# Kernel optimization log

Measured on AMD Instinct MI355X. Metric: run time of the kernel, lower is better.

Reference implementation:

```python
import jax, jax.numpy as jnp
import numpy as np

N, E = 50000, 800000
H, KC, EC, NH = 64, 64, 32, 4   # hidden, key, edge channels, heads
HPH, KPH = H // NH, KC // NH    # per-head value/key dims (16, 16)


def ssp(x):
    # ShiftedSoftplus
    return jax.nn.softplus(x) - jnp.log(2.0).astype(x.dtype)


def grouped_lin(x, w):
    # x: (N, NH, in_per_head), w: (NH, out_per_head, in_per_head)
    # equivalent to Conv1d(kernel=1, groups=NH, bias=False)
    return jnp.einsum('nhi,hoi->nho', x, w)


def lin(x, w, b):
    return x @ w.T + b


def segment_softmax(logits, seg, num_segments):
    # logits: (E, NH), seg: (E,)
    m = jax.ops.segment_max(logits, seg, num_segments=num_segments)
    m = jnp.where(jnp.isfinite(m), m, 0.0)
    e = jnp.exp(logits - m[seg])
    s = jax.ops.segment_sum(e, seg, num_segments=num_segments)
    return e / s[seg]


def setup_inputs() -> dict:
    key = jax.random.key(0)
    ks = jax.random.split(key, 24)
    sc = 0.05
    inp = {
        'x': jax.random.normal(ks[0], (N, H), jnp.float32),
        'edge_index': jax.random.randint(ks[1], (2, E), 0, N, jnp.int64),
        'edge_attr': jax.random.normal(ks[2], (E, EC), jnp.float32),
        # grouped 1x1 convs (block-diagonal linears), no bias
        'k_w': jax.random.normal(ks[3], (NH, KPH, HPH), jnp.float32) * sc,
        'q_w': jax.random.normal(ks[4], (NH, KPH, HPH), jnp.float32) * sc,
        'v_w': jax.random.normal(ks[5], (NH, HPH, HPH), jnp.float32) * sc,
        # weight_k_net: Linear(EC,KPH) -> ssp -> Linear(KPH,KPH)
        'wkn_w1': jax.random.normal(ks[6], (KPH, EC), jnp.float32) * sc,
        'wkn_b1': jnp.zeros((KPH,), jnp.float32),
        'wkn_w2': jax.random.normal(ks[7], (KPH, KPH), jnp.float32) * sc,
        'wkn_b2': jnp.zeros((KPH,), jnp.float32),
        'wkl_w': jax.random.normal(ks[8], (KPH, KPH), jnp.float32) * sc,
        'wkl_b': jnp.zeros((KPH,), jnp.float32),
        # weight_v_net: Linear(EC,HPH) -> ssp -> Linear(HPH,HPH)
        'wvn_w1': jax.random.normal(ks[9], (HPH, EC), jnp.float32) * sc,
        'wvn_b1': jnp.zeros((HPH,), jnp.float32),
        'wvn_w2': jax.random.normal(ks[10], (HPH, HPH), jnp.float32) * sc,
        'wvn_b2': jnp.zeros((HPH,), jnp.float32),
        'wvl_w': jax.random.normal(ks[11], (HPH, HPH), jnp.float32) * sc,
        'wvl_b': jnp.zeros((HPH,), jnp.float32),
        'cen_w': jax.random.normal(ks[12], (H, H), jnp.float32) * sc,
        'cen_b': jnp.zeros((H,), jnp.float32),
        'out_w': jax.random.normal(ks[13], (H, H), jnp.float32) * sc,
        'out_b': jnp.zeros((H,), jnp.float32),
    }
    return inp


def reference(x, edge_index, edge_attr, k_w, q_w, v_w,
              wkn_w1, wkn_b1, wkn_w2, wkn_b2, wkl_w, wkl_b,
              wvn_w1, wvn_b1, wvn_w2, wvn_b2, wvl_w, wvl_b,
              cen_w, cen_b, out_w, out_b):
    n = x.shape[0]
    row, col = edge_index[0], edge_index[1]
    xh = x.reshape(n, NH, HPH)                       # per-head split of channels
    h_keys = grouped_lin(xh, k_w)                    # (N, NH, KPH)
    h_queries = grouped_lin(xh, q_w)                 # (N, NH, KPH)
    h_values = grouped_lin(xh, v_w)                  # (N, NH, HPH)

    W_k = lin(ssp(lin(edge_attr, wkn_w1, wkn_b1)), wkn_w2, wkn_b2)   # (E, KPH)
    keys_j = lin(W_k[:, None, :] * h_keys[col], wkl_w, wkl_b)        # (E, NH, KPH)
    queries_i = h_queries[row]                                       # (E, NH, KPH)
    qk_ij = jnp.sum(queries_i * keys_j, axis=-1)                     # (E, NH)
    alpha = segment_softmax(qk_ij, row, n)                           # (E, NH)

    W_v = lin(ssp(lin(edge_attr, wvn_w1, wvn_b1)), wvn_w2, wvn_b2)   # (E, HPH)
    msg_j = lin(W_v[:, None, :] * h_values[col], wvl_w, wvl_b)       # (E, NH, HPH)
    msg_j = alpha[:, :, None] * msg_j
    aggr = jax.ops.segment_sum(msg_j, row, num_segments=n).reshape(n, H)

    out = lin(x, cen_w, cen_b) + aggr
    return lin(ssp(out), out_w, out_b)
```

## Files before the change

kernel.cpp:

```cpp
#include <hip/hip_runtime.h>
#include <math.h>
#include <stdint.h>

#define NN 50000
#define NE 800000
#define HD 64
#define ECH 32
#define NHEAD 4
#define NBLK 196
#define NEBLK (NE / 256)

static_assert(NE % 256 == 0, "edge kernel assumes full blocks");

typedef __attribute__((ext_vector_type(8))) short bf8;
typedef __attribute__((ext_vector_type(4))) float f32x4;
typedef __attribute__((ext_vector_type(2))) float v2f;
typedef __attribute__((ext_vector_type(2))) __bf16 v2bf;

__device__ __forceinline__ float ssp_f(float v) {
    return fmaxf(v, 0.0f) + log1pf(__expf(-fabsf(v))) - 0.69314718055994531f;
}
__device__ __forceinline__ float bf2f(uint32_t b) { return __uint_as_float(b << 16); }

__device__ __forceinline__ uint32_t cvt_pk_bf16(float lo, float hi) {
    v2f v = {lo, hi};
    v2bf b = __builtin_convertvector(v, v2bf);
    return __builtin_bit_cast(uint32_t, b);
}
__device__ __forceinline__ v2f bfpair(uint32_t p) {
    v2f r;
    r.x = __uint_as_float(p << 16);
    r.y = __uint_as_float(p & 0xffff0000u);
    return r;
}
__device__ __forceinline__ uint4 pack8c(const float* s) {
    uint4 r;
    r.x = cvt_pk_bf16(s[0], s[1]);
    r.y = cvt_pk_bf16(s[2], s[3]);
    r.z = cvt_pk_bf16(s[4], s[5]);
    r.w = cvt_pk_bf16(s[6], s[7]);
    return r;
}
__device__ __forceinline__ bf8 pack_bf8(float4 a, float4 b) {
    union { uint32_t u[4]; bf8 v; } r;
    r.u[0] = cvt_pk_bf16(a.x, a.y);
    r.u[1] = cvt_pk_bf16(a.z, a.w);
    r.u[2] = cvt_pk_bf16(b.x, b.y);
    r.u[3] = cvt_pk_bf16(b.z, b.w);
    return r.v;
}
__device__ __forceinline__ bf8 zero_bf8() {
    bf8 r;
    #pragma unroll
    for (int i = 0; i < 8; ++i) r[i] = 0;
    return r;
}

__global__ __launch_bounds__(256) void node_count_kernel(
    const float* __restrict__ x, const int* __restrict__ ei,
    const float* __restrict__ k_w, const float* __restrict__ q_w, const float* __restrict__ v_w,
    const float* __restrict__ wkl_w, const float* __restrict__ wkl_b,
    uint16_t* __restrict__ qtq, uint16_t* __restrict__ hkv,
    int* __restrict__ counts)
{
    atomicAdd(counts + ei[blockIdx.x * 256 + threadIdx.x], 1);

    if (blockIdx.x >= NBLK) return;
    __shared__ float skw[NHEAD * 256], sqw[NHEAD * 256], svw[NHEAD * 256];
    __shared__ float s_kl[256], s_klb[16];
    for (int i = threadIdx.x; i < NHEAD * 256; i += 256) {
        skw[i] = k_w[i]; sqw[i] = q_w[i]; svw[i] = v_w[i];
    }
    if (threadIdx.x < 256) s_kl[threadIdx.x] = wkl_w[threadIdx.x];
    if (threadIdx.x < 16) s_klb[threadIdx.x] = wkl_b[threadIdx.x];
    __syncthreads();
    int n = blockIdx.x * 256 + threadIdx.x;
    if (n >= NN) return;
    const float* xn = x + (size_t)n * HD;
    uint16_t* qrow = qtq + (size_t)n * 72;
    uint16_t* kvrow = hkv + (size_t)n * 128;
    float qbv[NHEAD];
    for (int h = 0; h < NHEAD; ++h) {
        v2f xr2[8];
        {
            const float4* xp = (const float4*)(xn + h * 16);
            #pragma unroll
            for (int j = 0; j < 4; ++j) {
                float4 t4 = xp[j];
                xr2[2 * j] = (v2f){t4.x, t4.y};
                xr2[2 * j + 1] = (v2f){t4.z, t4.w};
            }
        }
        float rq[16], rk[16], rv[16];
        for (int o = 0; o < 16; ++o) {
            const v2f* wq = (const v2f*)(sqw + h * 256 + o * 16);
            const v2f* wk = (const v2f*)(skw + h * 256 + o * 16);
            const v2f* wv = (const v2f*)(svw + h * 256 + o * 16);
            v2f sq = {0.f, 0.f}, sk = {0.f, 0.f}, sv = {0.f, 0.f};
            #pragma unroll
            for (int j = 0; j < 8; ++j) {
                sq += xr2[j] * wq[j];
                sk += xr2[j] * wk[j];
                sv += xr2[j] * wv[j];
            }
            rq[o] = sq.x + sq.y; rk[o] = sk.x + sk.y; rv[o] = sv.x + sv.y;
        }
        float rqt[16];
        #pragma unroll
        for (int ip = 0; ip < 8; ++ip) {
            v2f s2 = {0.f, 0.f};
            #pragma unroll
            for (int o = 0; o < 16; ++o) {
                v2f kl = *(const v2f*)(s_kl + o * 16 + 2 * ip);
                v2f q2 = {rq[o], rq[o]};
                s2 += q2 * kl;
            }
            rqt[2 * ip] = s2.x; rqt[2 * ip + 1] = s2.y;
        }
        float qbh = 0.f;
        #pragma unroll
        for (int o = 0; o < 16; ++o) qbh += rq[o] * s_klb[o];
        qbv[h] = qbh;

        uint4* oq = (uint4*)(qrow + h * 16);
        uint4* ok = (uint4*)(kvrow + h * 16);
        uint4* ov = (uint4*)(kvrow + 64 + h * 16);
        oq[0] = pack8c(rqt); oq[1] = pack8c(rqt + 8);
        ok[0] = pack8c(rk);  ok[1] = pack8c(rk + 8);
        ov[0] = pack8c(rv);  ov[1] = pack8c(rv + 8);
    }
    *(float4*)(qrow + 64) = *(float4*)&qbv[0];
}

__global__ __launch_bounds__(256) void scan_bsum_kernel(
    const int* __restrict__ counts, int* __restrict__ bsum)
{
    __shared__ int sd[256];
    int i = blockIdx.x * 256 + threadIdx.x;
    sd[threadIdx.x] = (i < NN) ? counts[i] : 0;
    __syncthreads();
    for (int s = 128; s > 0; s >>= 1) {
        if (threadIdx.x < (unsigned)s) sd[threadIdx.x] += sd[threadIdx.x + s];
        __syncthreads();
    }
    if (threadIdx.x == 0) bsum[blockIdx.x] = sd[0];
}

__global__ __launch_bounds__(256) void scan_top_kernel(int* __restrict__ bsum)
{
    __shared__ int tmp[256];
    int v = (threadIdx.x < NBLK) ? bsum[threadIdx.x] : 0;
    tmp[threadIdx.x] = v;
    __syncthreads();
    for (int d = 1; d < 256; d <<= 1) {
        int t = (threadIdx.x >= (unsigned)d) ? tmp[threadIdx.x - d] : 0;
        __syncthreads();
        tmp[threadIdx.x] += t;
        __syncthreads();
    }
    if (threadIdx.x < NBLK) bsum[threadIdx.x] = tmp[threadIdx.x] - v;
}

__global__ __launch_bounds__(256) void scan_final_kernel(
    const int* __restrict__ counts, const int* __restrict__ bsum,
    int* __restrict__ offsets, int* __restrict__ cursor)
{
    __shared__ int tmp[256];
    int i = blockIdx.x * 256 + threadIdx.x;
    int v = (i < NN) ? counts[i] : 0;
    tmp[threadIdx.x] = v;
    __syncthreads();
    for (int d = 1; d < 256; d <<= 1) {
        int t = (threadIdx.x >= (unsigned)d) ? tmp[threadIdx.x - d] : 0;
        __syncthreads();
        tmp[threadIdx.x] += t;
        __syncthreads();
    }
    int excl = tmp[threadIdx.x] - v + bsum[blockIdx.x];
    if (i < NN) { offsets[i] = excl; cursor[i] = excl; }
}

__global__ __launch_bounds__(256) void scatter_kernel(
    const int* __restrict__ ei, int* __restrict__ cursor,
    int* __restrict__ elist, int2* __restrict__ rc)
{
    int e = blockIdx.x * 256 + threadIdx.x;
    if (e >= NE) return;
    int r = ei[e];
    int c = ei[NE + e];
    int pos = atomicAdd(cursor + r, 1);
    elist[pos] = e;
    rc[pos] = make_int2(r, c);
}

__global__ __launch_bounds__(256) void edge_compute_kernel(
    const int* __restrict__ elist, const int2* __restrict__ rc,
    const float* __restrict__ ea,
    const float* __restrict__ wkn_w1, const float* __restrict__ wkn_b1,
    const float* __restrict__ wkn_w2, const float* __restrict__ wkn_b2,
    const float* __restrict__ wvn_w1, const float* __restrict__ wvn_b1,
    const float* __restrict__ wvn_w2, const float* __restrict__ wvn_b2,
    const uint16_t* __restrict__ qtq, const uint16_t* __restrict__ hkv,
    uint16_t* __restrict__ payload, float* __restrict__ wfac)
{
    __shared__ uint16_t s_trA[4][64][24];
    __shared__ uint16_t s_trB[4][64][24];

    const int w = threadIdx.x >> 6;
    const int L = threadIdx.x & 63;
    const int m = L & 15;
    const int g = L >> 4;
    const int ebase = blockIdx.x * 256 + w * 64;

    int eidv[4];
    int2 rcv[4];
    #pragma unroll
    for (int t = 0; t < 4; ++t) eidv[t] = elist[ebase + 16 * t + m];
    #pragma unroll
    for (int t = 0; t < 4; ++t) rcv[t] = rc[ebase + 16 * t + m];

    bf8 eaf[4];
    #pragma unroll
    for (int t = 0; t < 4; ++t) {
        const float* er = ea + (size_t)eidv[t] * ECH + 8 * g;
        eaf[t] = pack_bf8(*(const float4*)er, *(const float4*)(er + 4));
    }
    bf8 w1kf, w1vf, w2kf, w2vf;
    {
        const float* p = wkn_w1 + m * 32 + 8 * g;
        w1kf = pack_bf8(*(const float4*)p, *(const float4*)(p + 4));
        p = wvn_w1 + m * 32 + 8 * g;
        w1vf = pack_bf8(*(const float4*)p, *(const float4*)(p + 4));
        if (g < 2) {
            p = wkn_w2 + m * 16 + 8 * g;
            w2kf = pack_bf8(*(const float4*)p, *(const float4*)(p + 4));
            p = wvn_w2 + m * 16 + 8 * g;
            w2vf = pack_bf8(*(const float4*)p, *(const float4*)(p + 4));
        } else {
            w2kf = zero_bf8(); w2vf = zero_bf8();
        }
    }
    float4 b1k = *(const float4*)(wkn_b1 + 4 * g);
    float4 b1v = *(const float4*)(wvn_b1 + 4 * g);
    float4 b2k = *(const float4*)(wkn_b2 + 4 * g);
    float4 b2v = *(const float4*)(wvn_b2 + 4 * g);

    #pragma unroll
    for (int t = 0; t < 4; ++t) {
        f32x4 acc = {b1k.x, b1k.y, b1k.z, b1k.w};
        acc = __builtin_amdgcn_mfma_f32_16x16x32_bf16(w1kf, eaf[t], acc, 0, 0, 0);
        uint2 pk;
        pk.x = cvt_pk_bf16(ssp_f(acc[0]), ssp_f(acc[1]));
        pk.y = cvt_pk_bf16(ssp_f(acc[2]), ssp_f(acc[3]));
        *(uint2*)&s_trA[w][16 * t + m][4 * g] = pk;
    }
    bf8 l1k[4];
    #pragma unroll
    for (int t = 0; t < 4; ++t)
        l1k[t] = (g < 2) ? *(const bf8*)&s_trA[w][16 * t + m][8 * g] : zero_bf8();
    #pragma unroll
    for (int t = 0; t < 4; ++t) {
        f32x4 acc = {b1v.x, b1v.y, b1v.z, b1v.w};
        acc = __builtin_amdgcn_mfma_f32_16x16x32_bf16(w1vf, eaf[t], acc, 0, 0, 0);
        uint2 pk;
        pk.x = cvt_pk_bf16(ssp_f(acc[0]), ssp_f(acc[1]));
        pk.y = cvt_pk_bf16(ssp_f(acc[2]), ssp_f(acc[3]));
        *(uint2*)&s_trA[w][16 * t + m][4 * g] = pk;
    }
    bf8 l1v[4];
    #pragma unroll
    for (int t = 0; t < 4; ++t)
        l1v[t] = (g < 2) ? *(const bf8*)&s_trA[w][16 * t + m][8 * g] : zero_bf8();

    #pragma unroll
    for (int t = 0; t < 4; ++t) {
        f32x4 acc = {b2k.x, b2k.y, b2k.z, b2k.w};
        acc = __builtin_amdgcn_mfma_f32_16x16x32_bf16(w2kf, l1k[t], acc, 0, 0, 0);
        uint2 pk;
        pk.x = cvt_pk_bf16(acc[0], acc[1]);
        pk.y = cvt_pk_bf16(acc[2], acc[3]);
        *(uint2*)&s_trB[w][16 * t + m][4 * g] = pk;

        f32x4 accv = {b2v.x, b2v.y, b2v.z, b2v.w};
        accv = __builtin_amdgcn_mfma_f32_16x16x32_bf16(w2vf, l1v[t], accv, 0, 0, 0);
        uint2 pv;
        pv.x = cvt_pk_bf16(accv[0], accv[1]);
        pv.y = cvt_pk_bf16(accv[2], accv[3]);
        *(uint2*)&s_trA[w][16 * t + m][4 * g] = pv;
    }

    #pragma unroll
    for (int t = 0; t < 4; ++t) {
        const int E = ebase + 16 * t + m;
        const int row = rcv[t].x, col = rcv[t].y;

        uint32_t wk_u[8], wv_u[8];
        *(uint4*)&wk_u[0] = *(const uint4*)&s_trB[w][16 * t + m][0];
        *(uint4*)&wk_u[4] = *(const uint4*)&s_trB[w][16 * t + m][8];
        *(uint4*)&wv_u[0] = *(const uint4*)&s_trA[w][16 * t + m][0];
        *(uint4*)&wv_u[4] = *(const uint4*)&s_trA[w][16 * t + m][8];

        const uint16_t* qrow = qtq + (size_t)row * 72;
        const uint16_t* kvrow = hkv + (size_t)col * 128;
        uint32_t q_u[8], k_u[8], v_u[8];
        *(uint4*)&q_u[0] = *(const uint4*)(qrow + 16 * g);
        *(uint4*)&q_u[4] = *(const uint4*)(qrow + 16 * g + 8);
        *(uint4*)&k_u[0] = *(const uint4*)(kvrow + 16 * g);
        *(uint4*)&k_u[4] = *(const uint4*)(kvrow + 16 * g + 8);
        *(uint4*)&v_u[0] = *(const uint4*)(kvrow + 64 + 16 * g);
        *(uint4*)&v_u[4] = *(const uint4*)(kvrow + 64 + 16 * g + 8);

        v2f qk2 = {0.f, 0.f};
        #pragma unroll
        for (int i = 0; i < 8; ++i)
            qk2 += bfpair(q_u[i]) * (bfpair(wk_u[i]) * bfpair(k_u[i]));
        float qk = *(const float*)(qrow + 64 + 2 * g) + qk2.x + qk2.y;
        float wgt = __expf(qk);
        v2f wgt2 = {wgt, wgt};

        uint32_t po[8];
        #pragma unroll
        for (int i = 0; i < 8; ++i) {
            v2f o2 = (bfpair(wv_u[i]) * bfpair(v_u[i])) * wgt2;
            po[i] = cvt_pk_bf16(o2.x, o2.y);
        }
        uint4* pd = (uint4*)(payload + (size_t)E * HD + 16 * g);
        pd[0] = *(uint4*)&po[0];
        pd[1] = *(uint4*)&po[4];
        wfac[(size_t)E * NHEAD + g] = wgt;
    }
}

__global__ __launch_bounds__(256) void gather_finalize_kernel(
    const float* __restrict__ x,
    const uint16_t* __restrict__ payload, const float* __restrict__ wfac,
    const int* __restrict__ offsets, const int* __restrict__ counts,
    const float* __restrict__ wvl_w, const float* __restrict__ wvl_b,
    const float* __restrict__ cen_w, const float* __restrict__ cen_b,
    const float* __restrict__ out_w, const float* __restrict__ out_b,
    float* __restrict__ out)
{
    __shared__ float s_cw[4096], s_ow[4096];
    __shared__ float s_wvl[256], s_vlb[16];
    __shared__ float s_m[4][64], s_x[4][64], s_t[4][64];
    for (int idx = threadIdx.x; idx < 4096; idx += 256) {
        int o = idx & 63, i = idx >> 6;
        s_cw[i * 64 + o] = cen_w[o * 64 + i];
        s_ow[i * 64 + o] = out_w[o * 64 + i];
    }
    if (threadIdx.x < 256) s_wvl[threadIdx.x] = wvl_w[threadIdx.x];
    if (threadIdx.x < 16) s_vlb[threadIdx.x] = wvl_b[threadIdx.x];
    __syncthreads();

    int l = threadIdx.x >> 6;
    int L = threadIdx.x & 63;
    int q = L & 7;
    int g = L >> 3;
    int h = q >> 1;

    int n0 = blockIdx.x * 64 + l * 16;
    int pj = n0 + (L & 15);
    bool pvalid = pj < NN;
    int offv = 0, cntv = 0;
    if (L < 16) offv = pvalid ? offsets[pj] : 0;
    else if (L < 32) cntv = pvalid ? counts[pj] : 0;

    for (int t = 0; t < 16; ++t) {
        int n = n0 + t;
        bool valid = n < NN;
        int st = __shfl(offv, t);
        int deg = valid ? __shfl(cntv, 16 + t) : 0;
        float u[8] = {0.f, 0.f, 0.f, 0.f, 0.f, 0.f, 0.f, 0.f};
        float ds = 0.f;
        const uint16_t* pp = payload + (size_t)st * HD + 8 * q;
        const float* wp = wfac + (size_t)st * NHEAD + h;
        int iters = (deg + 7) >> 3;
        for (int i = 0; i < iters; ++i) {
            int e = 8 * i + g;
            if (e < deg) {
                uint4 pv = *(const uint4*)(pp + (size_t)e * HD);
                u[0] += bf2f(pv.x & 0xffffu); u[1] += bf2f(pv.x >> 16);
                u[2] += bf2f(pv.y & 0xffffu); u[3] += bf2f(pv.y >> 16);
                u[4] += bf2f(pv.z & 0xffffu); u[5] += bf2f(pv.z >> 16);
                u[6] += bf2f(pv.w & 0xffffu); u[7] += bf2f(pv.w >> 16);
                ds += wp[(size_t)e * NHEAD];
            }
        }
        #pragma unroll
        for (int s = 8; s < 64; s <<= 1) {
            #pragma unroll
            for (int j = 0; j < 8; ++j) u[j] += __shfl_xor(u[j], s);
            ds += __shfl_xor(ds, s);
        }
        if (g == 0) {
            float inv = (deg > 0) ? (1.f / ds) : 0.f;
            float r0[4] = {u[0] * inv, u[1] * inv, u[2] * inv, u[3] * inv};
            float r1[4] = {u[4] * inv, u[5] * inv, u[6] * inv, u[7] * inv};
            *(float4*)&s_m[l][8 * q] = *(float4*)r0;
            *(float4*)&s_m[l][8 * q + 4] = *(float4*)r1;
        }
        s_x[l][L] = valid ? x[(size_t)n * HD + L] : 0.f;

        int c = L, hh = c >> 4;
        float aggr = 0.f;
        if (deg > 0) {
            int o = c & 15;
            float s = s_vlb[o];
            #pragma unroll
            for (int i = 0; i < 16; ++i) s += s_m[l][hh * 16 + i] * s_wvl[o * 16 + i];
            aggr = s;
        }
        float sc = cen_b[c];
        #pragma unroll 8
        for (int i = 0; i < 64; ++i) sc += s_x[l][i] * s_cw[i * 64 + c];
        sc += aggr;
        s_t[l][c] = ssp_f(sc);
        float so = out_b[c];
        #pragma unroll 8
        for (int i = 0; i < 64; ++i) so += s_t[l][i] * s_ow[i * 64 + c];
        if (valid) out[(size_t)n * HD + c] = so;
    }
}

extern "C" void kernel_launch(void* const* d_in, const int* in_sizes, int n_in,
                              void* d_out, int out_size, void* d_ws, size_t ws_size,
                              hipStream_t stream)
{
    const float* x      = (const float*)d_in[0];
    const int*   ei     = (const int*)d_in[1];
    const float* ea     = (const float*)d_in[2];
    const float* k_w    = (const float*)d_in[3];
    const float* q_w    = (const float*)d_in[4];
    const float* v_w    = (const float*)d_in[5];
    const float* wkn_w1 = (const float*)d_in[6];
    const float* wkn_b1 = (const float*)d_in[7];
    const float* wkn_w2 = (const float*)d_in[8];
    const float* wkn_b2 = (const float*)d_in[9];
    const float* wkl_w  = (const float*)d_in[10];
    const float* wkl_b  = (const float*)d_in[11];
    const float* wvn_w1 = (const float*)d_in[12];
    const float* wvn_b1 = (const float*)d_in[13];
    const float* wvn_w2 = (const float*)d_in[14];
    const float* wvn_b2 = (const float*)d_in[15];
    const float* wvl_w  = (const float*)d_in[16];
    const float* wvl_b  = (const float*)d_in[17];
    const float* cen_w  = (const float*)d_in[18];
    const float* cen_b  = (const float*)d_in[19];
    const float* out_w  = (const float*)d_in[20];
    const float* out_b  = (const float*)d_in[21];
    float* out = (float*)d_out;

    float* wfac  = (float*)d_ws;
    uint16_t* qtq = (uint16_t*)(wfac + (size_t)NE * NHEAD);
    uint16_t* hkv = qtq + (size_t)NN * 72;
    uint16_t* payload = hkv + (size_t)NN * 128;
    int2* rc     = (int2*)(payload + (size_t)NE * HD);
    int* elist   = (int*)(rc + (size_t)NE);
    int* counts  = elist + NE;
    int* bsum    = counts + NN;
    int* offsets = bsum + 256;
    int* cursor  = offsets + NN;

    hipMemsetAsync(counts, 0, (size_t)NN * sizeof(int), stream);
    node_count_kernel<<<NEBLK, 256, 0, stream>>>(
        x, ei, k_w, q_w, v_w, wkl_w, wkl_b, qtq, hkv, counts);
    scan_bsum_kernel<<<NBLK, 256, 0, stream>>>(counts, bsum);
    scan_top_kernel<<<1, 256, 0, stream>>>(bsum);
    scan_final_kernel<<<NBLK, 256, 0, stream>>>(counts, bsum, offsets, cursor);
    scatter_kernel<<<NEBLK, 256, 0, stream>>>(ei, cursor, elist, rc);
    edge_compute_kernel<<<NEBLK, 256, 0, stream>>>(
        elist, rc, ea, wkn_w1, wkn_b1, wkn_w2, wkn_b2,
        wvn_w1, wvn_b1, wvn_w2, wvn_b2,
        qtq, hkv, payload, wfac);
    gather_finalize_kernel<<<(NN + 63) / 64, 256, 0, stream>>>(
        x, payload, wfac, offsets, counts,
        wvl_w, wvl_b, cen_w, cen_b, out_w, out_b, out);
}
```

Before: 474.7 us.

## Split gather_finalize into a wave-per-node gather kernel and separate finalize kernel

```diff
diff --git a/kernel.cpp b/kernel.cpp
--- a/kernel.cpp
+++ b/kernel.cpp
@@ -331,91 +331,110 @@
     }
 }
 
-__global__ __launch_bounds__(256) void gather_finalize_kernel(
-    const float* __restrict__ x,
+__global__ __launch_bounds__(256) void gather_kernel(
     const uint16_t* __restrict__ payload, const float* __restrict__ wfac,
     const int* __restrict__ offsets, const int* __restrict__ counts,
+    float* __restrict__ mout)
+{
+    const int n = (blockIdx.x * 256 + threadIdx.x) >> 6;
+    if (n >= NN) return;
+    const int L = threadIdx.x & 63;
+    const int q = L & 7;
+    const int g = L >> 3;
+    const int h = q >> 1;
+
+    const int st = offsets[n];
+    const int deg = counts[n];
+
+    v2f u2[4] = {{0.f,0.f},{0.f,0.f},{0.f,0.f},{0.f,0.f}};
+    float ds = 0.f;
+    const uint16_t* pp = payload + (size_t)st * HD + 8 * q;
+    const float* wp = wfac + (size_t)st * NHEAD + h;
+    const int iters = (deg + 7) >> 3;
+    for (int i = 0; i < iters; i += 2) {
+        const int e0 = 8 * i + g;
+        const int e1 = e0 + 8;
+        if (e0 < deg) {
+            uint4 pv = *(const uint4*)(pp + (size_t)e0 * HD);
+            u2[0] += bfpair(pv.x); u2[1] += bfpair(pv.y);
+            u2[2] += bfpair(pv.z); u2[3] += bfpair(pv.w);
+            ds += wp[(size_t)e0 * NHEAD];
+        }
+        if (e1 < deg) {
+            uint4 pv = *(const uint4*)(pp + (size_t)e1 * HD);
+            u2[0] += bfpair(pv.x); u2[1] += bfpair(pv.y);
+            u2[2] += bfpair(pv.z); u2[3] += bfpair(pv.w);
+            ds += wp[(size_t)e1 * NHEAD];
+        }
+    }
+    #pragma unroll
+    for (int s = 8; s < 64; s <<= 1) {
+        #pragma unroll
+        for (int j = 0; j < 4; ++j) {
+            u2[j].x += __shfl_xor(u2[j].x, s);
+            u2[j].y += __shfl_xor(u2[j].y, s);
+        }
+        ds += __shfl_xor(ds, s);
+    }
+    if (g == 0) {
+        float inv = (deg > 0) ? (1.f / ds) : 0.f;
+        float r0[4] = {u2[0].x * inv, u2[0].y * inv, u2[1].x * inv, u2[1].y * inv};
+        float r1[4] = {u2[2].x * inv, u2[2].y * inv, u2[3].x * inv, u2[3].y * inv};
+        float* mr = mout + (size_t)n * HD + 8 * q;
+        *(float4*)mr = *(float4*)r0;
+        *(float4*)(mr + 4) = *(float4*)r1;
+    }
+}
+
+__global__ __launch_bounds__(256) void finalize_kernel(
+    const float* __restrict__ x, const float* __restrict__ m,
+    const int* __restrict__ counts,
     const float* __restrict__ wvl_w, const float* __restrict__ wvl_b,
     const float* __restrict__ cen_w, const float* __restrict__ cen_b,
     const float* __restrict__ out_w, const float* __restrict__ out_b,
     float* __restrict__ out)
 {
     __shared__ float s_cw[4096], s_ow[4096];
-    __shared__ float s_wvl[256], s_vlb[16];
-    __shared__ float s_m[4][64], s_x[4][64], s_t[4][64];
+    __shared__ float s_x[4][64], s_m[4][64], s_t[4][64];
     for (int idx = threadIdx.x; idx < 4096; idx += 256) {
         int o = idx & 63, i = idx >> 6;
         s_cw[i * 64 + o] = cen_w[o * 64 + i];
         s_ow[i * 64 + o] = out_w[o * 64 + i];
     }
-    if (threadIdx.x < 256) s_wvl[threadIdx.x] = wvl_w[threadIdx.x];
-    if (threadIdx.x < 16) s_vlb[threadIdx.x] = wvl_b[threadIdx.x];
     __syncthreads();
 
-    int l = threadIdx.x >> 6;
-    int L = threadIdx.x & 63;
-    int q = L & 7;
-    int g = L >> 3;
-    int h = q >> 1;
-
-    int n0 = blockIdx.x * 64 + l * 16;
-    int pj = n0 + (L & 15);
-    bool pvalid = pj < NN;
-    int offv = 0, cntv = 0;
-    if (L < 16) offv = pvalid ? offsets[pj] : 0;
-    else if (L < 32) cntv = pvalid ? counts[pj] : 0;
-
+    const int l = threadIdx.x >> 6;
+    const int c = threadIdx.x & 63;
+    const int hh = c >> 4;
+
+    float wvlr[16];
+    #pragma unroll
+    for (int i = 0; i < 16; ++i) wvlr[i] = wvl_w[(c & 15) * 16 + i];
+    const float vlb = wvl_b[c & 15];
+    const float cb = cen_b[c];
+    const float ob = out_b[c];
+
+    const int n0 = blockIdx.x * 64 + l * 16;
     for (int t = 0; t < 16; ++t) {
-        int n = n0 + t;
-        bool valid = n < NN;
-        int st = __shfl(offv, t);
-        int deg = valid ? __shfl(cntv, 16 + t) : 0;
-        float u[8] = {0.f, 0.f, 0.f, 0.f, 0.f, 0.f, 0.f, 0.f};
-        float ds = 0.f;
-        const uint16_t* pp = payload + (size_t)st * HD + 8 * q;
-        const float* wp = wfac + (size_t)st * NHEAD + h;
-        int iters = (deg + 7) >> 3;
-        for (int i = 0; i < iters; ++i) {
-            int e = 8 * i + g;
-            if (e < deg) {
-                uint4 pv = *(const uint4*)(pp + (size_t)e * HD);
-                u[0] += bf2f(pv.x & 0xffffu); u[1] += bf2f(pv.x >> 16);
-                u[2] += bf2f(pv.y & 0xffffu); u[3] += bf2f(pv.y >> 16);
-                u[4] += bf2f(pv.z & 0xffffu); u[5] += bf2f(pv.z >> 16);
-                u[6] += bf2f(pv.w & 0xffffu); u[7] += bf2f(pv.w >> 16);
-                ds += wp[(size_t)e * NHEAD];
-            }
-        }
-        #pragma unroll
-        for (int s = 8; s < 64; s <<= 1) {
-            #pragma unroll
-            for (int j = 0; j < 8; ++j) u[j] += __shfl_xor(u[j], s);
-            ds += __shfl_xor(ds, s);
-        }
-        if (g == 0) {
-            float inv = (deg > 0) ? (1.f / ds) : 0.f;
-            float r0[4] = {u[0] * inv, u[1] * inv, u[2] * inv, u[3] * inv};
-            float r1[4] = {u[4] * inv, u[5] * inv, u[6] * inv, u[7] * inv};
-            *(float4*)&s_m[l][8 * q] = *(float4*)r0;
-            *(float4*)&s_m[l][8 * q + 4] = *(float4*)r1;
-        }
-        s_x[l][L] = valid ? x[(size_t)n * HD + L] : 0.f;
-
-        int c = L, hh = c >> 4;
+        const int n = n0 + t;
+        const bool valid = n < NN;
+        const int deg = valid ? counts[n] : 0;
+        s_x[l][c] = valid ? x[(size_t)n * HD + c] : 0.f;
+        s_m[l][c] = valid ? m[(size_t)n * HD + c] : 0.f;
+
         float aggr = 0.f;
         if (deg > 0) {
-            int o = c & 15;
-            float s = s_vlb[o];
+            float s = vlb;
             #pragma unroll
-            for (int i = 0; i < 16; ++i) s += s_m[l][hh * 16 + i] * s_wvl[o * 16 + i];
+            for (int i = 0; i < 16; ++i) s += s_m[l][hh * 16 + i] * wvlr[i];
             aggr = s;
         }
-        float sc = cen_b[c];
+        float sc = cb;
         #pragma unroll 8
         for (int i = 0; i < 64; ++i) sc += s_x[l][i] * s_cw[i * 64 + c];
         sc += aggr;
         s_t[l][c] = ssp_f(sc);
-        float so = out_b[c];
+        float so = ob;
         #pragma unroll 8
         for (int i = 0; i < 64; ++i) so += s_t[l][i] * s_ow[i * 64 + c];
         if (valid) out[(size_t)n * HD + c] = so;
@@ -460,6 +479,7 @@
     int* bsum    = counts + NN;
     int* offsets = bsum + 256;
     int* cursor  = offsets + NN;
+    float* mbuf  = (float*)hkv;
 
     hipMemsetAsync(counts, 0, (size_t)NN * sizeof(int), stream);
     node_count_kernel<<<NEBLK, 256, 0, stream>>>(
@@ -472,7 +492,8 @@
         elist, rc, ea, wkn_w1, wkn_b1, wkn_w2, wkn_b2,
         wvn_w1, wvn_b1, wvn_w2, wvn_b2,
         qtq, hkv, payload, wfac);
-    gather_finalize_kernel<<<(NN + 63) / 64, 256, 0, stream>>>(
-        x, payload, wfac, offsets, counts,
-        wvl_w, wvl_b, cen_w, cen_b, out_w, out_b, out);
-}
+    gather_kernel<<<(NN * 64) / 256, 256, 0, stream>>>(
+        payload, wfac, offsets, counts, mbuf);
+    finalize_kernel<<<(NN + 63) / 64, 256, 0, stream>>>(
+        x, mbuf, counts, wvl_w, wvl_b, cen_w, cen_b, out_w, out_b, out);
+}
```

New measurement: 465.9 us. No clear change (-1.9%).
